# Kernel optimization log

Hardware: AMD Instinct MI355X
Metric: run time of the kernel (lower is better)

## Reference

```python
import jax, jax.numpy as jnp
import numpy as np

B, T, C = 16, 1024, 32
PATCH_SIZE = 4
NB_PATCHES = 400
STRETCH = 8
K = PATCH_SIZE * C          # patch_size * num_channels = 128
S_MAIN = T // STRETCH       # 128 strided steps for the main layer
P_TOP = max(int(0.15 * NB_PATCHES), PATCH_SIZE - 1)  # 60 ontop patches


def setup_inputs() -> dict:
    key = jax.random.key(0)
    k0, k1, k2, k3, k4 = jax.random.split(key, 5)
    x = jax.random.normal(k0, (B, T, C), dtype=jnp.float32)
    # flattened (time*C + channel) gather indices, stand-in for the
    # precomputed random (time, channel) pairs used by tf.gather_nd
    idx_main = jax.random.randint(k1, (S_MAIN, NB_PATCHES, K), 0, T * C, dtype=jnp.int32)
    idx_top = jax.random.randint(k2, (T, P_TOP, K), 0, T * C, dtype=jnp.int32)
    W_main = jax.random.normal(k3, (S_MAIN, NB_PATCHES, K), dtype=jnp.float32) * 0.05
    b_main = jnp.zeros((S_MAIN, NB_PATCHES), dtype=jnp.float32)
    W_top = jax.random.normal(k4, (T, P_TOP, K), dtype=jnp.float32) * 0.05
    b_top = jnp.zeros((T, P_TOP), dtype=jnp.float32)
    return {"x": x, "W_main": W_main, "b_main": b_main,
            "W_top": W_top, "b_top": b_top,
            "idx_main": idx_main, "idx_top": idx_top}


def reference(x, W_main, b_main, W_top, b_top, idx_main, idx_top):
    # x: [B, T, C] -> flatten time/channel plane for gather (== gather_nd on [T, C, B])
    Bsz, Tlen, Cch = x.shape
    flat = x.reshape(Bsz, Tlen * Cch)                      # [B, T*C]
    # main strided patches: [B, S_MAIN, NB_PATCHES, K]
    Mm = jnp.take(flat, idx_main.reshape(-1), axis=1).reshape(Bsz, *idx_main.shape)
    out_main = jax.nn.leaky_relu(
        jnp.einsum('bspk,spk->bsp', Mm, W_main) + b_main, 0.3)  # [B, S_MAIN, P]
    # upsample strided steps back to full sequence (tf_repeat along time)
    stretch = Tlen // idx_main.shape[0]
    out_main = jnp.repeat(out_main, stretch, axis=1)            # [B, T, P]
    # ontop patches at every step: [B, T, P_TOP, K]
    Mt = jnp.take(flat, idx_top.reshape(-1), axis=1).reshape(Bsz, *idx_top.shape)
    out_top = jax.nn.leaky_relu(
        jnp.einsum('btpk,tpk->btp', Mt, W_top) + b_top, 0.3)    # [B, T, P_TOP]
    return jnp.concatenate([out_main, out_top], axis=-1)       # [B, T, P + P_TOP]
```

## Files before the change

### kernel.cpp

```cpp
#include <hip/hip_runtime.h>

#define B_SZ    16
#define T_LEN   1024
#define C_CH    32
#define TC      (T_LEN * C_CH)
#define S_MAIN  128
#define NB_P    400
#define P_TOP   60
#define OUT_CH  (NB_P + P_TOP)

typedef float        v4f __attribute__((ext_vector_type(4)));
typedef int          v4i __attribute__((ext_vector_type(4)));
typedef unsigned int v4u __attribute__((ext_vector_type(4)));

__device__ __forceinline__ unsigned short f32_to_bf16_rne(float f) {
    unsigned int u = __float_as_uint(f);
    unsigned int r = u + 0x7fffu + ((u >> 16) & 1u);
    return (unsigned short)(r >> 16);
}

__global__ __launch_bounds__(256) void transpose_pack(const float* __restrict__ x,
                                                      unsigned int* __restrict__ xb) {
    const int i = blockIdx.x * 256 + threadIdx.x;
    unsigned int u[8];
    #pragma unroll
    for (int k = 0; k < 8; ++k) {
        float v0 = __builtin_nontemporal_load(x + (size_t)(2 * k)     * TC + i);
        float v1 = __builtin_nontemporal_load(x + (size_t)(2 * k + 1) * TC + i);
        u[k] = (unsigned int)f32_to_bf16_rne(v0) |
               ((unsigned int)f32_to_bf16_rne(v1) << 16);
    }
    v4u a = { u[0], u[1], u[2], u[3] };
    v4u b = { u[4], u[5], u[6], u[7] };
    v4u* out = (v4u*)xb;
    out[(size_t)i * 2]     = a;
    out[(size_t)i * 2 + 1] = b;
}

template <int NPAIR_P, int NROWS, bool TO_WS>
__global__ __launch_bounds__(256, 4) void patch_v3(
    const v4u*   __restrict__ xb4,
    const int*   __restrict__ idx,
    const float* __restrict__ W,
    const float* __restrict__ bias,
    float*       __restrict__ dst)
{
    __shared__ int   s_idx[16][128];
    __shared__ float s_w[16][128];
    const int wave = threadIdx.x >> 6;
    const int lane = threadIdx.x & 63;
    const int pairBase = blockIdx.x * 16 + wave * 4;

    #pragma unroll
    for (int q = 0; q < 4; ++q) {
        const int pr = pairBase + q;
        if (lane < 32) {
            v4i t = __builtin_nontemporal_load((const v4i*)idx + (size_t)pr * 32 + lane);
            *(v4i*)&s_idx[wave * 4 + q][lane * 4] = t;
        } else {
            v4f t = __builtin_nontemporal_load((const v4f*)W + (size_t)pr * 32 + (lane - 32));
            *(v4f*)&s_w[wave * 4 + q][(lane - 32) * 4] = t;
        }
    }

    const int j  = lane >> 1;
    const int bh = lane & 1;

    float acc[4][8];
    #pragma unroll
    for (int q = 0; q < 4; ++q)
        #pragma unroll
        for (int k = 0; k < 8; ++k) acc[q][k] = 0.f;

    float bv[4];

    #pragma unroll
    for (int q = 0; q < 4; ++q) {
        bv[q] = bias[pairBase + q];
        #pragma unroll
        for (int g = 0; g < 4; ++g) {
            const int   ix = s_idx[wave * 4 + q][g * 32 + j];
            const float wt = s_w [wave * 4 + q][g * 32 + j];
            const v4u gv = xb4[(size_t)ix * 2 + bh];
            acc[q][0] += __uint_as_float(gv.x << 16)          * wt;
            acc[q][1] += __uint_as_float(gv.x & 0xffff0000u)  * wt;
            acc[q][2] += __uint_as_float(gv.y << 16)          * wt;
            acc[q][3] += __uint_as_float(gv.y & 0xffff0000u)  * wt;
            acc[q][4] += __uint_as_float(gv.z << 16)          * wt;
            acc[q][5] += __uint_as_float(gv.z & 0xffff0000u)  * wt;
            acc[q][6] += __uint_as_float(gv.w << 16)          * wt;
            acc[q][7] += __uint_as_float(gv.w & 0xffff0000u)  * wt;
        }
    }

    #pragma unroll
    for (int q = 0; q < 4; ++q)
        #pragma unroll
        for (int m = 2; m <= 32; m <<= 1)
            #pragma unroll
            for (int k = 0; k < 8; ++k)
                acc[q][k] += __shfl_xor(acc[q][k], m);

    if (j == 0) {
        #pragma unroll
        for (int q = 0; q < 4; ++q) {
            const int pr  = pairBase + q;
            const int row = pr / NPAIR_P;
            const int p   = pr - row * NPAIR_P;
            #pragma unroll
            for (int k = 0; k < 8; ++k) {
                const int b = bh * 8 + k;
                float val = acc[q][k] + bv[q];
                val = (val > 0.f) ? val : 0.3f * val;
                if (TO_WS) {
                    dst[((size_t)b * NROWS + row) * NPAIR_P + p] = val;
                } else {
                    __builtin_nontemporal_store(
                        val, &dst[((size_t)b * T_LEN + row) * OUT_CH + NB_P + p]);
                }
            }
        }
    }
}

__global__ __launch_bounds__(256) void upsample_main(const float* __restrict__ ws_main,
                                                     float* __restrict__ out) {
    const int o4 = blockIdx.x * 256 + threadIdx.x;
    const int row = o4 / 100;
    const int col = o4 - row * 100;
    const int b = row >> 10;
    const int t = row & 1023;
    const int s = t >> 3;
    const v4f v = ((const v4f*)ws_main)[((size_t)b * S_MAIN + s) * 100 + col];
    __builtin_nontemporal_store(v, &((v4f*)out)[(size_t)row * 115 + col]);
}

extern "C" void kernel_launch(void* const* d_in, const int* in_sizes, int n_in,
                              void* d_out, int out_size, void* d_ws, size_t ws_size,
                              hipStream_t stream) {
    const float* x      = (const float*)d_in[0];
    const float* W_main = (const float*)d_in[1];
    const float* b_main = (const float*)d_in[2];
    const float* W_top  = (const float*)d_in[3];
    const float* b_top  = (const float*)d_in[4];
    const int*  idx_main = (const int*)d_in[5];
    const int*  idx_top  = (const int*)d_in[6];
    float* out = (float*)d_out;

    unsigned int* xb   = (unsigned int*)d_ws;
    float* ws_main     = (float*)((char*)d_ws + (size_t)TC * 16 * 2);

    transpose_pack<<<TC / 256, 256, 0, stream>>>(x, xb);

    patch_v3<NB_P, S_MAIN, true>
        <<<(S_MAIN * NB_P) / 16, 256, 0, stream>>>((const v4u*)xb, idx_main, W_main, b_main, ws_main);

    patch_v3<P_TOP, T_LEN, false>
        <<<(T_LEN * P_TOP) / 16, 256, 0, stream>>>((const v4u*)xb, idx_top, W_top, b_top, out);

    upsample_main<<<(B_SZ * T_LEN * 100) / 256, 256, 0, stream>>>(ws_main, out);
}
```

Measured before the change: 274.2 us.

## Map one patch per wave with direct register loads instead of LDS staging

```diff
diff --git a/kernel.cpp b/kernel.cpp
--- a/kernel.cpp
+++ b/kernel.cpp
@@ -19,14 +19,18 @@
     return (unsigned short)(r >> 16);
 }
 
+__device__ __forceinline__ float leaky(float v) {
+    return (v > 0.f) ? v : 0.3f * v;
+}
+
 __global__ __launch_bounds__(256) void transpose_pack(const float* __restrict__ x,
                                                       unsigned int* __restrict__ xb) {
     const int i = blockIdx.x * 256 + threadIdx.x;
     unsigned int u[8];
     #pragma unroll
     for (int k = 0; k < 8; ++k) {
-        float v0 = __builtin_nontemporal_load(x + (size_t)(2 * k)     * TC + i);
-        float v1 = __builtin_nontemporal_load(x + (size_t)(2 * k + 1) * TC + i);
+        float v0 = x[(size_t)(2 * k)     * TC + i];
+        float v1 = x[(size_t)(2 * k + 1) * TC + i];
         u[k] = (unsigned int)f32_to_bf16_rne(v0) |
                ((unsigned int)f32_to_bf16_rne(v1) << 16);
     }
@@ -38,86 +42,60 @@
 }
 
 template <int NPAIR_P, int NROWS, bool TO_WS>
-__global__ __launch_bounds__(256, 4) void patch_v3(
+__global__ __launch_bounds__(256) void patch_nt(
     const v4u*   __restrict__ xb4,
     const int*   __restrict__ idx,
     const float* __restrict__ W,
     const float* __restrict__ bias,
     float*       __restrict__ dst)
 {
-    __shared__ int   s_idx[16][128];
-    __shared__ float s_w[16][128];
     const int wave = threadIdx.x >> 6;
     const int lane = threadIdx.x & 63;
-    const int pairBase = blockIdx.x * 16 + wave * 4;
+    const int pair = blockIdx.x * 4 + wave;
+    const int j    = lane >> 1;
+    const int bh   = lane & 1;
 
+    const v4i iv = __builtin_nontemporal_load((const v4i*)(idx + (size_t)pair * 128) + j);
+    const v4f wv = __builtin_nontemporal_load((const v4f*)(W   + (size_t)pair * 128) + j);
+
+    float acc[8];
     #pragma unroll
-    for (int q = 0; q < 4; ++q) {
-        const int pr = pairBase + q;
-        if (lane < 32) {
-            v4i t = __builtin_nontemporal_load((const v4i*)idx + (size_t)pr * 32 + lane);
-            *(v4i*)&s_idx[wave * 4 + q][lane * 4] = t;
-        } else {
-            v4f t = __builtin_nontemporal_load((const v4f*)W + (size_t)pr * 32 + (lane - 32));
-            *(v4f*)&s_w[wave * 4 + q][(lane - 32) * 4] = t;
-        }
-    }
+    for (int k = 0; k < 8; ++k) acc[k] = 0.f;
 
-    const int j  = lane >> 1;
-    const int bh = lane & 1;
-
-    float acc[4][8];
+    const int ixs[4] = { iv.x, iv.y, iv.z, iv.w };
+    const float wts[4] = { wv.x, wv.y, wv.z, wv.w };
     #pragma unroll
-    for (int q = 0; q < 4; ++q)
-        #pragma unroll
-        for (int k = 0; k < 8; ++k) acc[q][k] = 0.f;
-
-    float bv[4];
-
-    #pragma unroll
-    for (int q = 0; q < 4; ++q) {
-        bv[q] = bias[pairBase + q];
-        #pragma unroll
-        for (int g = 0; g < 4; ++g) {
-            const int   ix = s_idx[wave * 4 + q][g * 32 + j];
-            const float wt = s_w [wave * 4 + q][g * 32 + j];
-            const v4u gv = xb4[(size_t)ix * 2 + bh];
-            acc[q][0] += __uint_as_float(gv.x << 16)          * wt;
-            acc[q][1] += __uint_as_float(gv.x & 0xffff0000u)  * wt;
-            acc[q][2] += __uint_as_float(gv.y << 16)          * wt;
-            acc[q][3] += __uint_as_float(gv.y & 0xffff0000u)  * wt;
-            acc[q][4] += __uint_as_float(gv.z << 16)          * wt;
-            acc[q][5] += __uint_as_float(gv.z & 0xffff0000u)  * wt;
-            acc[q][6] += __uint_as_float(gv.w << 16)          * wt;
-            acc[q][7] += __uint_as_float(gv.w & 0xffff0000u)  * wt;
-        }
+    for (int m = 0; m < 4; ++m) {
+        const v4u gv = __builtin_nontemporal_load(xb4 + (size_t)ixs[m] * 2 + bh);
+        const float wt = wts[m];
+        acc[0] += __uint_as_float(gv.x << 16)         * wt;
+        acc[1] += __uint_as_float(gv.x & 0xffff0000u) * wt;
+        acc[2] += __uint_as_float(gv.y << 16)         * wt;
+        acc[3] += __uint_as_float(gv.y & 0xffff0000u) * wt;
+        acc[4] += __uint_as_float(gv.z << 16)         * wt;
+        acc[5] += __uint_as_float(gv.z & 0xffff0000u) * wt;
+        acc[6] += __uint_as_float(gv.w << 16)         * wt;
+        acc[7] += __uint_as_float(gv.w & 0xffff0000u) * wt;
     }
 
     #pragma unroll
-    for (int q = 0; q < 4; ++q)
+    for (int m = 2; m <= 32; m <<= 1)
         #pragma unroll
-        for (int m = 2; m <= 32; m <<= 1)
-            #pragma unroll
-            for (int k = 0; k < 8; ++k)
-                acc[q][k] += __shfl_xor(acc[q][k], m);
+        for (int k = 0; k < 8; ++k)
+            acc[k] += __shfl_xor(acc[k], m);
 
     if (j == 0) {
+        const float bv = bias[pair];
+        const int row = pair / NPAIR_P;
+        const int p   = pair - row * NPAIR_P;
         #pragma unroll
-        for (int q = 0; q < 4; ++q) {
-            const int pr  = pairBase + q;
-            const int row = pr / NPAIR_P;
-            const int p   = pr - row * NPAIR_P;
-            #pragma unroll
-            for (int k = 0; k < 8; ++k) {
-                const int b = bh * 8 + k;
-                float val = acc[q][k] + bv[q];
-                val = (val > 0.f) ? val : 0.3f * val;
-                if (TO_WS) {
-                    dst[((size_t)b * NROWS + row) * NPAIR_P + p] = val;
-                } else {
-                    __builtin_nontemporal_store(
-                        val, &dst[((size_t)b * T_LEN + row) * OUT_CH + NB_P + p]);
-                }
+        for (int k = 0; k < 8; ++k) {
+            const int b = bh * 8 + k;
+            const float val = leaky(acc[k] + bv);
+            if (TO_WS) {
+                dst[((size_t)b * NROWS + row) * NPAIR_P + p] = val;
+            } else {
+                dst[((size_t)b * T_LEN + row) * OUT_CH + NB_P + p] = val;
             }
         }
     }
@@ -132,7 +110,7 @@
     const int t = row & 1023;
     const int s = t >> 3;
     const v4f v = ((const v4f*)ws_main)[((size_t)b * S_MAIN + s) * 100 + col];
-    __builtin_nontemporal_store(v, &((v4f*)out)[(size_t)row * 115 + col]);
+    ((v4f*)out)[(size_t)row * 115 + col] = v;
 }
 
 extern "C" void kernel_launch(void* const* d_in, const int* in_sizes, int n_in,
@@ -152,11 +130,11 @@
 
     transpose_pack<<<TC / 256, 256, 0, stream>>>(x, xb);
 
-    patch_v3<NB_P, S_MAIN, true>
-        <<<(S_MAIN * NB_P) / 16, 256, 0, stream>>>((const v4u*)xb, idx_main, W_main, b_main, ws_main);
+    patch_nt<NB_P, S_MAIN, true>
+        <<<(S_MAIN * NB_P) / 4, 256, 0, stream>>>((const v4u*)xb, idx_main, W_main, b_main, ws_main);
 
-    patch_v3<P_TOP, T_LEN, false>
-        <<<(T_LEN * P_TOP) / 16, 256, 0, stream>>>((const v4u*)xb, idx_top, W_top, b_top, out);
+    patch_nt<P_TOP, T_LEN, false>
+        <<<(T_LEN * P_TOP) / 4, 256, 0, stream>>>((const v4u*)xb, idx_top, W_top, b_top, out);
 
     upsample_main<<<(B_SZ * T_LEN * 100) / 256, 256, 0, stream>>>(ws_main, out);
 }
```

Measured after the change: 293.9 us. +7.2%, slower.
